# Kernel tuning notes

Hardware: AMD Instinct MI355X
Metric: run time of the kernel (lower is better)

The kernel has to match this reference:

```python
import jax, jax.numpy as jnp
import numpy as np

HEADS = 4
DIM_HEAD = 32
SCALE = DIM_HEAD ** -0.5
EPS = 1e-5


def setup_inputs() -> dict:
    key = jax.random.key(0)
    ks = jax.random.split(key, 4)
    x = jax.random.normal(ks[0], (8, 64, 32, 32, 32), dtype=jnp.float32)
    w_qkv = jax.random.normal(ks[1], (384, 64), dtype=jnp.float32) * 0.05
    w_out = jax.random.normal(ks[2], (64, 128), dtype=jnp.float32) * 0.05
    b_out = jax.random.normal(ks[3], (64,), dtype=jnp.float32) * 0.05
    gamma = jnp.ones((64,), dtype=jnp.float32)
    beta = jnp.zeros((64,), dtype=jnp.float32)
    return {"x": x, "w_qkv": w_qkv, "w_out": w_out, "b_out": b_out,
            "gamma": gamma, "beta": beta}


def reference(x, w_qkv, w_out, b_out, gamma, beta):
    b, c, l, h, w = x.shape
    n = l * h * w
    xf = x.reshape(b, c, n)
    # 1x1 Conv3d (no bias) == channel matmul
    qkv = jnp.einsum('oc,bcn->bon', w_qkv, xf)            # [b, 3*H*D, n]
    q, k, v = jnp.split(qkv, 3, axis=1)
    def to_heads(t):
        return t.reshape(b, HEADS, DIM_HEAD, n)            # [b, H, D, n]
    q, k, v = to_heads(q), to_heads(k), to_heads(v)
    q = jax.nn.softmax(q, axis=2) * SCALE                  # softmax over head dim
    k = jax.nn.softmax(k, axis=3)                          # softmax over tokens
    context = jnp.einsum('bhdn,bhen->bhde', k, v)          # [b, H, D, D]
    out = jnp.einsum('bhde,bhdn->bhen', context, q)        # [b, H, D, n]
    out = out.reshape(b, HEADS * DIM_HEAD, n)
    # to_out: 1x1 Conv3d with bias, then GroupNorm(1, dim)
    out = jnp.einsum('oc,bcn->bon', w_out, out) + b_out[None, :, None]
    mu = out.mean(axis=(1, 2), keepdims=True)
    var = out.var(axis=(1, 2), keepdims=True)
    out = (out - mu) * jax.lax.rsqrt(var + EPS)
    out = out * gamma[None, :, None] + beta[None, :, None]
    return out.reshape(b, c, l, h, w)
```

## Files before the change

kernel.cpp:

```cpp
#include <hip/hip_runtime.h>

typedef __bf16 bf16;
typedef __bf16 bf16x4 __attribute__((ext_vector_type(4)));
typedef __bf16 bf16x8 __attribute__((ext_vector_type(8)));
typedef float f32x4 __attribute__((ext_vector_type(4)));

#define NTOK 32768
#define SCALE_F 0.17677669529663689f

__global__ __launch_bounds__(256) void k1_ctx(const float* __restrict__ x,
    const float* __restrict__ wqkv, float* __restrict__ ctx, float* __restrict__ s1)
{
  const int b = blockIdx.y, chunk = blockIdx.x;
  const int t = threadIdx.x, w = t>>6, l = t&63, lr = l&15, lg = l>>4;
  __shared__ bf16 xT[64*72];
  __shared__ bf16 ek[128*72];
  __shared__ bf16 vl[128*72];

  bf16x8 bw[4][2];
  #pragma unroll
  for (int ct=0;ct<4;ct++)
    #pragma unroll
    for (int ks=0;ks<2;ks++){
      const float* src = wqkv + (128 + w*64 + ct*16 + lr)*64 + ks*32 + lg*8;
      #pragma unroll
      for (int j=0;j<8;j++) bw[ct][ks][j] = (bf16)src[j];
    }
  bf16x8 ones;
  #pragma unroll
  for (int j=0;j<8;j++) ones[j] = (bf16)1.0f;

  f32x4 ctxa[2][2]; f32x4 s1a[2];
  #pragma unroll
  for (int i=0;i<2;i++){
    s1a[i] = f32x4{0.f,0.f,0.f,0.f};
    #pragma unroll
    for (int j=0;j<2;j++) ctxa[i][j] = f32x4{0.f,0.f,0.f,0.f};
  }
  const float* xb = x + (long)b*64*NTOK;
  bf16* dst = (w<2) ? ek : vl;
  const int chb = (w&1)*64;
  const bool isk = (w<2);
  const int sn = t&63, cg16 = (t>>6)*16;

  bf16x8 t0, t1;
  {
    const int n0 = chunk*256;
    #pragma unroll
    for (int i=0;i<8;i++) t0[i] = (bf16)xb[(long)(cg16+i)*NTOK + n0 + sn];
    #pragma unroll
    for (int i=0;i<8;i++) t1[i] = (bf16)xb[(long)(cg16+8+i)*NTOK + n0 + sn];
  }

  for (int s=0; s<4; s++) {
    *(bf16x8*)&xT[sn*72 + cg16]     = t0;
    *(bf16x8*)&xT[sn*72 + cg16 + 8] = t1;
    __syncthreads();
    if (s+1 < 4){
      const int n0 = chunk*256 + (s+1)*64;
      #pragma unroll
      for (int i=0;i<8;i++) t0[i] = (bf16)xb[(long)(cg16+i)*NTOK + n0 + sn];
      #pragma unroll
      for (int i=0;i<8;i++) t1[i] = (bf16)xb[(long)(cg16+8+i)*NTOK + n0 + sn];
    }
    f32x4 acc[4][4];
    #pragma unroll
    for (int rt=0;rt<4;rt++)
      #pragma unroll
      for (int ct=0;ct<4;ct++) acc[rt][ct] = f32x4{0.f,0.f,0.f,0.f};
    #pragma unroll
    for (int ks=0;ks<2;ks++){
      bf16x8 af[4];
      #pragma unroll
      for (int rt=0;rt<4;rt++)
        af[rt] = *(const bf16x8*)&xT[(rt*16+lr)*72 + ks*32 + lg*8];
      #pragma unroll
      for (int rt=0;rt<4;rt++)
        #pragma unroll
        for (int ct=0;ct<4;ct++)
          acc[rt][ct] = __builtin_amdgcn_mfma_f32_16x16x32_bf16(af[rt], bw[ct][ks], acc[rt][ct], 0,0,0);
    }
    #pragma unroll
    for (int ct=0;ct<4;ct++){
      const int row = chb + ct*16 + lr;
      #pragma unroll
      for (int rt=0;rt<4;rt++){
        bf16x4 p;
        #pragma unroll
        for (int ri=0;ri<4;ri++){
          const float v = acc[rt][ct][ri];
          p[ri] = isk ? (bf16)__expf(v) : (bf16)v;
        }
        *(bf16x4*)&dst[row*72 + rt*16 + lg*4] = p;
      }
    }
    __syncthreads();
    #pragma unroll
    for (int ks=0;ks<2;ks++){
      bf16x8 bd[2];
      #pragma unroll
      for (int cd=0;cd<2;cd++)
        bd[cd] = *(const bf16x8*)&ek[(w*32 + cd*16 + lr)*72 + ks*32 + lg*8];
      #pragma unroll
      for (int re=0;re<2;re++){
        bf16x8 a = *(const bf16x8*)&vl[(w*32 + re*16 + lr)*72 + ks*32 + lg*8];
        #pragma unroll
        for (int cd=0;cd<2;cd++)
          ctxa[re][cd] = __builtin_amdgcn_mfma_f32_16x16x32_bf16(a, bd[cd], ctxa[re][cd], 0,0,0);
      }
      #pragma unroll
      for (int cd=0;cd<2;cd++)
        s1a[cd] = __builtin_amdgcn_mfma_f32_16x16x32_bf16(ones, bd[cd], s1a[cd], 0,0,0);
    }
  }
  float* cp = ctx + ((long)b*4 + w)*1024;
  #pragma unroll
  for (int re=0;re<2;re++)
    #pragma unroll
    for (int cd=0;cd<2;cd++)
      #pragma unroll
      for (int ri=0;ri<4;ri++){
        const int e = re*16 + lg*4 + ri, d = cd*16 + lr;
        atomicAdd(&cp[e*32 + d], ctxa[re][cd][ri]);
      }
  if (lg==0){
    #pragma unroll
    for (int cd=0;cd<2;cd++)
      atomicAdd(&s1[(long)b*128 + w*32 + cd*16 + lr], s1a[cd][0]);
  }
}

__global__ __launch_bounds__(256) void k2_w2(const float* __restrict__ ctx,
    const float* __restrict__ s1, const float* __restrict__ wout, bf16* __restrict__ W2)
{
  const int b = blockIdx.y, h = blockIdx.x, t = threadIdx.x;
  __shared__ float cs[1024];
  __shared__ float s1s[32];
  {
    f32x4 p4 = *(const f32x4*)(ctx + ((long)b*4 + h)*1024 + t*4);
    *(f32x4*)&cs[t*4] = p4;
  }
  if (t < 32) s1s[t] = s1[(long)b*128 + h*32 + t];
  __syncthreads();
  const int d = t & 31;
  const float rinv = SCALE_F / s1s[d];
  #pragma unroll
  for (int oi=0; oi<8; oi++){
    const int o = (t>>5)*8 + oi;
    float acc = 0.f;
    #pragma unroll
    for (int e=0;e<32;e++) acc += wout[o*128 + h*32 + e] * cs[e*32 + d];
    W2[((long)b*64 + o)*128 + h*32 + d] = (bf16)(acc * rinv);
  }
}

#define K3T 4
__global__ __launch_bounds__(256,2) void k3_y(const float* __restrict__ x,
    const float* __restrict__ wqkv, const bf16* __restrict__ W2g,
    const float* __restrict__ bout, bf16* __restrict__ ybf, float* __restrict__ yacc)
{
  const int b = blockIdx.y, blk = blockIdx.x;
  const int t = threadIdx.x, w = t>>6, l = t&63, lr = l&15, lg = l>>4;
  __shared__ bf16 W2s[64*136];
  __shared__ bf16 xT[64*72];
  __shared__ bf16 qs[64*136];
  __shared__ float red[8];
  const float* xb = x + (long)b*64*NTOK;
  bf16* yb = ybf + (long)b*64*NTOK;

  bf16x8 qfr[2][2];
  #pragma unroll
  for (int rt=0;rt<2;rt++)
    #pragma unroll
    for (int ks=0;ks<2;ks++){
      const float* src = wqkv + (w*32 + rt*16 + lr)*64 + ks*32 + lg*8;
      #pragma unroll
      for (int j=0;j<8;j++) qfr[rt][ks][j] = (bf16)src[j];
    }
  {
    const bf16* src = W2g + (long)b*8192 + t*32;
    const int o = t>>2, c0 = (t&3)*32;
    #pragma unroll
    for (int k=0;k<4;k++)
      *(bf16x8*)&W2s[o*136 + c0 + k*8] = *(const bf16x8*)(src + k*8);
  }
  float boutr[16];
  #pragma unroll
  for (int rt=0;rt<4;rt++)
    #pragma unroll
    for (int ri=0;ri<4;ri++) boutr[rt*4+ri] = bout[rt*16 + lg*4 + ri];

  const int sn = t&63, cg16 = (t>>6)*16;
  bf16x8 t0, t1;
  {
    const int n0 = blk*K3T*64;
    #pragma unroll
    for (int i=0;i<8;i++) t0[i] = (bf16)xb[(long)(cg16+i)*NTOK + n0 + sn];
    #pragma unroll
    for (int i=0;i<8;i++) t1[i] = (bf16)xb[(long)(cg16+8+i)*NTOK + n0 + sn];
  }
  float sum=0.f, ss=0.f;

  #pragma unroll
  for (int ti=0; ti<K3T; ti++){
    const int n0 = (blk*K3T + ti)*64;
    *(bf16x8*)&xT[sn*72 + cg16]     = t0;
    *(bf16x8*)&xT[sn*72 + cg16 + 8] = t1;
    __syncthreads();
    if (ti+1 < K3T){
      const int nn0 = n0 + 64;
      #pragma unroll
      for (int i=0;i<8;i++) t0[i] = (bf16)xb[(long)(cg16+i)*NTOK + nn0 + sn];
      #pragma unroll
      for (int i=0;i<8;i++) t1[i] = (bf16)xb[(long)(cg16+8+i)*NTOK + nn0 + sn];
    }
    f32x4 qa[2][4];
    #pragma unroll
    for (int rt=0;rt<2;rt++)
      #pragma unroll
      for (int ct=0;ct<4;ct++) qa[rt][ct] = f32x4{0.f,0.f,0.f,0.f};
    #pragma unroll
    for (int ks=0;ks<2;ks++){
      bf16x8 bfr[4];
      #pragma unroll
      for (int ct=0;ct<4;ct++)
        bfr[ct] = *(const bf16x8*)&xT[(ct*16+lr)*72 + ks*32 + lg*8];
      #pragma unroll
      for (int rt=0;rt<2;rt++)
        #pragma unroll
        for (int ct=0;ct<4;ct++)
          qa[rt][ct] = __builtin_amdgcn_mfma_f32_16x16x32_bf16(qfr[rt][ks], bfr[ct], qa[rt][ct], 0,0,0);
    }
    #pragma unroll
    for (int ct=0;ct<4;ct++){
      float e[2][4]; float p = 0.f;
      #pragma unroll
      for (int rt=0;rt<2;rt++)
        #pragma unroll
        for (int ri=0;ri<4;ri++){ e[rt][ri] = __expf(qa[rt][ct][ri]); p += e[rt][ri]; }
      p += __shfl_xor(p, 16, 64);
      p += __shfl_xor(p, 32, 64);
      const float rinv = 1.f/p;
      const int nn = ct*16 + lr;
      #pragma unroll
      for (int rt=0;rt<2;rt++){
        bf16x4 pk;
        #pragma unroll
        for (int ri=0;ri<4;ri++) pk[ri] = (bf16)(e[rt][ri]*rinv);
        *(bf16x4*)&qs[nn*136 + w*32 + rt*16 + lg*4] = pk;
      }
    }
    __syncthreads();
    f32x4 ya[4];
    #pragma unroll
    for (int rt=0;rt<4;rt++) ya[rt] = f32x4{0.f,0.f,0.f,0.f};
    #pragma unroll
    for (int ks=0;ks<4;ks++){
      bf16x8 bq = *(const bf16x8*)&qs[(w*16+lr)*136 + ks*32 + lg*8];
      #pragma unroll
      for (int rt=0;rt<4;rt++){
        bf16x8 a = *(const bf16x8*)&W2s[(rt*16+lr)*136 + ks*32 + lg*8];
        ya[rt] = __builtin_amdgcn_mfma_f32_16x16x32_bf16(a, bq, ya[rt], 0,0,0);
      }
    }
    #pragma unroll
    for (int rt=0;rt<4;rt++)
      #pragma unroll
      for (int ri=0;ri<4;ri++){
        const int o = rt*16 + lg*4 + ri;
        const float val = ya[rt][ri] + boutr[rt*4+ri];
        sum += val; ss += val*val;
        yb[(long)o*NTOK + n0 + w*16 + lr] = (bf16)val;
      }
    __syncthreads();
  }
  #pragma unroll
  for (int off=1; off<64; off<<=1){
    sum += __shfl_xor(sum, off, 64);
    ss  += __shfl_xor(ss,  off, 64);
  }
  if (l==0){ red[w*2] = sum; red[w*2+1] = ss; }
  __syncthreads();
  if (t==0){
    atomicAdd(&yacc[b*2],   red[0]+red[2]+red[4]+red[6]);
    atomicAdd(&yacc[b*2+1], red[1]+red[3]+red[5]+red[7]);
  }
}

__global__ __launch_bounds__(256) void k4_norm(const bf16* __restrict__ ybf,
    const float* __restrict__ yacc, const float* __restrict__ gamma,
    const float* __restrict__ beta, float* __restrict__ out)
{
  const long idx = ((long)blockIdx.x*256 + threadIdx.x)*8;
  const int b = (int)(idx >> 21);
  const int c = (int)((idx >> 15) & 63);
  const float inv_n = 1.f/2097152.f;
  const float mu  = yacc[b*2]*inv_n;
  const float inv = rsqrtf(yacc[b*2+1]*inv_n - mu*mu + 1e-5f);
  const float g = gamma[c]*inv;
  const float be = beta[c] - mu*g;
  bf16x8 v8 = *(const bf16x8*)(ybf + idx);
  f32x4 o0, o1;
  #pragma unroll
  for (int j=0;j<4;j++){ o0[j] = (float)v8[j]*g + be; o1[j] = (float)v8[4+j]*g + be; }
  *(f32x4*)(out + idx)     = o0;
  *(f32x4*)(out + idx + 4) = o1;
}

extern "C" void kernel_launch(void* const* d_in, const int* in_sizes, int n_in,
                              void* d_out, int out_size, void* d_ws, size_t ws_size,
                              hipStream_t stream) {
  const float* x     = (const float*)d_in[0];
  const float* wqkv  = (const float*)d_in[1];
  const float* wout  = (const float*)d_in[2];
  const float* bout  = (const float*)d_in[3];
  const float* gamma = (const float*)d_in[4];
  const float* beta  = (const float*)d_in[5];
  float* out = (float*)d_out;
  char* ws = (char*)d_ws;
  if (ws_size < 33820736u) return;

  float* ctx  = (float*)(ws + 0);
  float* s1   = (float*)(ws + 131072);
  float* yacc = (float*)(ws + 135168);
  bf16*  W2   = (bf16*) (ws + 135232);
  bf16*  ybf  = (bf16*) (ws + 266304);

  hipMemsetAsync(ws, 0, 135232, stream);
  k1_ctx <<<dim3(128,8), 256, 0, stream>>>(x, wqkv, ctx, s1);
  k2_w2  <<<dim3(4,8),   256, 0, stream>>>(ctx, s1, wout, W2);
  k3_y   <<<dim3(128,8), 256, 0, stream>>>(x, wqkv, W2, bout, ybf, yacc);
  k4_norm<<<8192,        256, 0, stream>>>(ybf, yacc, gamma, beta, out);
}
```

Baseline: 115.1 us.

## Defer q-softmax normalization to per-head MFMA row sums in k3

The q softmax denominator is no longer computed with exps, shuffles and a reciprocal before packing. Instead, unnormalized exp(q) goes into shared memory, and the per-head column sums come from an extra MFMA against a ones vector. The output projection is then split per head and rescaled by the reciprocal sums. Separately, each block now covers 512 tokens (8 tiles, not unrolled) with half the grid, to amortize setup. Costs are four times the accumulator registers and an extra MFMA per head, which could hurt occupancy, plus the risk of bf16 overflow from storing unnormalized exps.

```diff
diff --git a/kernel.cpp b/kernel.cpp
--- a/kernel.cpp
+++ b/kernel.cpp
@@ -154,7 +154,6 @@
   }
 }
 
-#define K3T 4
 __global__ __launch_bounds__(256,2) void k3_y(const float* __restrict__ x,
     const float* __restrict__ wqkv, const bf16* __restrict__ W2g,
     const float* __restrict__ bout, bf16* __restrict__ ybf, float* __restrict__ yacc)
@@ -189,11 +188,14 @@
   for (int rt=0;rt<4;rt++)
     #pragma unroll
     for (int ri=0;ri<4;ri++) boutr[rt*4+ri] = bout[rt*16 + lg*4 + ri];
+  bf16x8 ones;
+  #pragma unroll
+  for (int j=0;j<8;j++) ones[j] = (bf16)1.0f;
 
   const int sn = t&63, cg16 = (t>>6)*16;
   bf16x8 t0, t1;
   {
-    const int n0 = blk*K3T*64;
+    const int n0 = blk*512;
     #pragma unroll
     for (int i=0;i<8;i++) t0[i] = (bf16)xb[(long)(cg16+i)*NTOK + n0 + sn];
     #pragma unroll
@@ -201,13 +203,12 @@
   }
   float sum=0.f, ss=0.f;
 
-  #pragma unroll
-  for (int ti=0; ti<K3T; ti++){
-    const int n0 = (blk*K3T + ti)*64;
+  for (int ti=0; ti<8; ti++){
+    const int n0 = blk*512 + ti*64;
     *(bf16x8*)&xT[sn*72 + cg16]     = t0;
     *(bf16x8*)&xT[sn*72 + cg16 + 8] = t1;
     __syncthreads();
-    if (ti+1 < K3T){
+    if (ti+1 < 8){
       const int nn0 = n0 + 64;
       #pragma unroll
       for (int i=0;i<8;i++) t0[i] = (bf16)xb[(long)(cg16+i)*NTOK + nn0 + sn];
@@ -233,42 +234,44 @@
     }
     #pragma unroll
     for (int ct=0;ct<4;ct++){
-      float e[2][4]; float p = 0.f;
-      #pragma unroll
-      for (int rt=0;rt<2;rt++)
-        #pragma unroll
-        for (int ri=0;ri<4;ri++){ e[rt][ri] = __expf(qa[rt][ct][ri]); p += e[rt][ri]; }
-      p += __shfl_xor(p, 16, 64);
-      p += __shfl_xor(p, 32, 64);
-      const float rinv = 1.f/p;
       const int nn = ct*16 + lr;
       #pragma unroll
       for (int rt=0;rt<2;rt++){
         bf16x4 pk;
         #pragma unroll
-        for (int ri=0;ri<4;ri++) pk[ri] = (bf16)(e[rt][ri]*rinv);
+        for (int ri=0;ri<4;ri++) pk[ri] = (bf16)__expf(qa[rt][ct][ri]);
         *(bf16x4*)&qs[nn*136 + w*32 + rt*16 + lg*4] = pk;
       }
     }
     __syncthreads();
-    f32x4 ya[4];
-    #pragma unroll
-    for (int rt=0;rt<4;rt++) ya[rt] = f32x4{0.f,0.f,0.f,0.f};
-    #pragma unroll
-    for (int ks=0;ks<4;ks++){
-      bf16x8 bq = *(const bf16x8*)&qs[(w*16+lr)*136 + ks*32 + lg*8];
+    f32x4 ya[4][4]; f32x4 sa[4];
+    #pragma unroll
+    for (int h=0;h<4;h++){
+      sa[h] = f32x4{0.f,0.f,0.f,0.f};
+      #pragma unroll
+      for (int rt=0;rt<4;rt++) ya[h][rt] = f32x4{0.f,0.f,0.f,0.f};
+    }
+    #pragma unroll
+    for (int h=0;h<4;h++){
+      bf16x8 bq = *(const bf16x8*)&qs[(w*16+lr)*136 + h*32 + lg*8];
+      sa[h] = __builtin_amdgcn_mfma_f32_16x16x32_bf16(ones, bq, sa[h], 0,0,0);
       #pragma unroll
       for (int rt=0;rt<4;rt++){
-        bf16x8 a = *(const bf16x8*)&W2s[(rt*16+lr)*136 + ks*32 + lg*8];
-        ya[rt] = __builtin_amdgcn_mfma_f32_16x16x32_bf16(a, bq, ya[rt], 0,0,0);
-      }
-    }
+        bf16x8 a = *(const bf16x8*)&W2s[(rt*16+lr)*136 + h*32 + lg*8];
+        ya[h][rt] = __builtin_amdgcn_mfma_f32_16x16x32_bf16(a, bq, ya[h][rt], 0,0,0);
+      }
+    }
+    float rinvh[4];
+    #pragma unroll
+    for (int h=0;h<4;h++) rinvh[h] = 1.f / sa[h][0];
     #pragma unroll
     for (int rt=0;rt<4;rt++)
       #pragma unroll
       for (int ri=0;ri<4;ri++){
         const int o = rt*16 + lg*4 + ri;
-        const float val = ya[rt][ri] + boutr[rt*4+ri];
+        const float val = ya[0][rt][ri]*rinvh[0] + ya[1][rt][ri]*rinvh[1]
+                        + ya[2][rt][ri]*rinvh[2] + ya[3][rt][ri]*rinvh[3]
+                        + boutr[rt*4+ri];
         sum += val; ss += val*val;
         yb[(long)o*NTOK + n0 + w*16 + lr] = (bf16)val;
       }
@@ -329,6 +332,6 @@
   hipMemsetAsync(ws, 0, 135232, stream);
   k1_ctx <<<dim3(128,8), 256, 0, stream>>>(x, wqkv, ctx, s1);
   k2_w2  <<<dim3(4,8),   256, 0, stream>>>(ctx, s1, wout, W2);
-  k3_y   <<<dim3(128,8), 256, 0, stream>>>(x, wqkv, W2, bout, ybf, yacc);
+  k3_y   <<<dim3(64,8),  256, 0, stream>>>(x, wqkv, W2, bout, ybf, yacc);
   k4_norm<<<8192,        256, 0, stream>>>(ybf, yacc, gamma, beta, out);
 }
```

After: 116.5 us. No clear change (+1.2%).
